# Optimization experiments

Hardware: AMD Instinct MI355X
Metric: run time of the kernel (lower is better)

## Reference

```python
import jax, jax.numpy as jnp
import numpy as np

N = 50000      # nodes
E = 800000     # edges (before self-loops)
DIN = 128
DH = 16        # per-head channels, layer 1
H = 8          # heads, layer 1
DOUT = 128     # layer 2 output (heads=1)
EDIM = 8       # edge_attr dim (unused by math: edge_dim=None in GATConv)
EPS_BN = 1e-5
NEG_SLOPE = 0.2


def _gat_conv(x, edge_index, W, a_src, a_dst, bias, heads, ch):
    """PyG GATConv (concat=True, add_self_loops=True, edge_dim=None)."""
    n = x.shape[0]
    loop = jnp.arange(n, dtype=edge_index.dtype)
    src = jnp.concatenate([edge_index[0], loop])  # [E+N]
    dst = jnp.concatenate([edge_index[1], loop])
    h = (x @ W).reshape(n, heads, ch)             # [N,H,C]
    s_src = jnp.einsum('nhc,hc->nh', h, a_src)    # [N,H]
    s_dst = jnp.einsum('nhc,hc->nh', h, a_dst)
    e = jax.nn.leaky_relu(s_src[src] + s_dst[dst], NEG_SLOPE)  # [E+N,H]
    # segment softmax over incoming edges of each dst node
    m = jax.ops.segment_max(e, dst, num_segments=n)
    ex = jnp.exp(e - m[dst])
    den = jax.ops.segment_sum(ex, dst, num_segments=n)
    alpha = ex / (den[dst] + 1e-16)               # [E+N,H]
    out = jax.ops.segment_sum(alpha[:, :, None] * h[src], dst, num_segments=n)
    return out.reshape(n, heads * ch) + bias


def _bn_selu(x, gamma, beta):
    # BatchNorm1d in training mode (batch statistics, biased variance) + SELU.
    mu = x.mean(axis=0)
    var = x.var(axis=0)
    xn = (x - mu) * jax.lax.rsqrt(var + EPS_BN)
    return jax.nn.selu(gamma * xn + beta)


def setup_inputs() -> dict:
    key = jax.random.key(0)
    ks = jax.random.split(key, 12)
    x = jax.random.normal(ks[0], (N, DIN), jnp.float32)
    edge_index = jax.random.randint(ks[1], (2, E), 0, N, jnp.int32)
    edge_attr = jax.random.normal(ks[2], (E, EDIM), jnp.float32)
    W1 = jax.random.normal(ks[3], (DIN, H * DH), jnp.float32) / np.sqrt(DIN)
    a_src1 = jax.random.normal(ks[4], (H, DH), jnp.float32) / np.sqrt(DH)
    a_dst1 = jax.random.normal(ks[5], (H, DH), jnp.float32) / np.sqrt(DH)
    b1 = jnp.zeros((H * DH,), jnp.float32)
    g1 = jnp.ones((H * DH,), jnp.float32)
    beta1 = jnp.zeros((H * DH,), jnp.float32)
    W2 = jax.random.normal(ks[6], (H * DH, DOUT), jnp.float32) / np.sqrt(H * DH)
    a_src2 = jax.random.normal(ks[7], (1, DOUT), jnp.float32) / np.sqrt(DOUT)
    a_dst2 = jax.random.normal(ks[8], (1, DOUT), jnp.float32) / np.sqrt(DOUT)
    b2 = jnp.zeros((DOUT,), jnp.float32)
    g2 = jnp.ones((DOUT,), jnp.float32)
    beta2 = jnp.zeros((DOUT,), jnp.float32)
    return dict(x=x, edge_index=edge_index, edge_attr=edge_attr,
                W1=W1, a_src1=a_src1, a_dst1=a_dst1, b1=b1, g1=g1, beta1=beta1,
                W2=W2, a_src2=a_src2, a_dst2=a_dst2, b2=b2, g2=g2, beta2=beta2)


def reference(x, edge_index, edge_attr,
              W1, a_src1, a_dst1, b1, g1, beta1,
              W2, a_src2, a_dst2, b2, g2, beta2):
    # edge_attr is unused: GATConv built with edge_dim=None ignores edge features.
    h = _gat_conv(x, edge_index, W1, a_src1, a_dst1, b1, H, DH)   # [N, H*DH]
    h = _bn_selu(h, g1, beta1)                                    # dropout = identity (eval)
    h = _gat_conv(h, edge_index, W2, a_src2, a_dst2, b2, 1, DOUT) # [N, DOUT]
    h = _bn_selu(h, g2, beta2)
    return h
```

## Files before the change

kernel.cpp:

```cpp
#include <hip/hip_runtime.h>

#define SELU_SCALE 1.0507009873554805f
#define SELU_ALPHA 1.6732632423543772f

typedef __attribute__((ext_vector_type(8))) short short8;
typedef __attribute__((ext_vector_type(4))) float f32x4;

#define BCAP 20480

static __device__ __forceinline__ float leaky02(float v) {
  return v > 0.0f ? v : 0.2f * v;
}

static __device__ __forceinline__ ushort f2bf(float f) {
  uint b = __float_as_uint(f);
  return (ushort)((b + 0x7fffu + ((b >> 16) & 1u)) >> 16);
}
static __device__ __forceinline__ float bf2f(ushort u) {
  return __uint_as_float(((uint)u) << 16);
}

static __device__ __forceinline__ float selu_f(float y) {
  return y > 0.f ? SELU_SCALE * y : SELU_SCALE * SELU_ALPHA * (__expf(y) - 1.f);
}

__global__ __launch_bounds__(256) void pack_kernel(const float* __restrict__ W1,
                                                   const float* __restrict__ W2,
                                                   ushort* __restrict__ Wp1,
                                                   ushort* __restrict__ Wp2) {
  int idx = blockIdx.x * 256 + threadIdx.x;
  const float* W = (idx < 16384) ? W1 : W2;
  ushort* Wp = (idx < 16384) ? Wp1 : Wp2;
  int t = idx & 16383;
  int b = t & 7, i = (t >> 3) & 15, g = (t >> 7) & 3, kt = (t >> 9) & 3, ct = t >> 11;
  int k = kt * 32 + g * 8 + b, col = ct * 16 + i;
  Wp[t] = f2bf(W[k * 128 + col]);
}

template <int HEADS, bool BN>
__global__ __launch_bounds__(256) void gemm_mfma_kernel(
    const float* __restrict__ X, const ushort* __restrict__ Wp, ushort* __restrict__ H,
    const float* __restrict__ asr, const float* __restrict__ adt,
    float* __restrict__ ssrc, float* __restrict__ sdst, int n,
    const float* __restrict__ stats, const float* __restrict__ gamma,
    const float* __restrict__ beta) {
  __shared__ float sc[128], sh[128];
  if (BN) {
    int t = threadIdx.x;
    if (t < 128) {
      float invN = 1.0f / (float)n;
      float mu = stats[t] * invN;
      float var = stats[128 + t] * invN - mu * mu;
      float rs = rsqrtf(var + 1e-5f);
      float s = gamma[t] * rs;
      sc[t] = s;
      sh[t] = beta[t] - s * mu;
    }
    __syncthreads();
  }
  const int tid = threadIdx.x;
  const int w = tid >> 6, l = tid & 63;
  const int lj = l & 15, lg = l >> 4;
  const int row = blockIdx.x * 64 + w * 16 + lj;
  const bool rowok = row < n;
  const float* xrow = X + (size_t)row * 128;

  f32x4 acc[8];
#pragma unroll
  for (int ct = 0; ct < 8; ++ct) acc[ct] = (f32x4){0.f, 0.f, 0.f, 0.f};

#pragma unroll
  for (int kt = 0; kt < 4; ++kt) {
    const int k0 = kt * 32 + lg * 8;
    float4 xa = make_float4(0.f, 0.f, 0.f, 0.f), xb = xa;
    if (rowok) {
      xa = *(const float4*)(xrow + k0);
      xb = *(const float4*)(xrow + k0 + 4);
    }
    float xv[8] = {xa.x, xa.y, xa.z, xa.w, xb.x, xb.y, xb.z, xb.w};
    if (BN) {
#pragma unroll
      for (int b = 0; b < 8; ++b) xv[b] = selu_f(xv[b] * sc[k0 + b] + sh[k0 + b]);
    }
    short8 bx;
#pragma unroll
    for (int b = 0; b < 8; ++b) bx[b] = (short)f2bf(xv[b]);
#pragma unroll
    for (int ct = 0; ct < 8; ++ct) {
      short8 af = *(const short8*)(Wp + ((((ct * 4 + kt) * 4 + lg) * 16 + lj) << 3));
      acc[ct] = __builtin_amdgcn_mfma_f32_16x16x32_bf16(af, bx, acc[ct], 0, 0, 0);
    }
  }

  if (rowok) {
#pragma unroll
    for (int ct = 0; ct < 8; ++ct) {
      ushort4 h4;
      h4.x = f2bf(acc[ct][0]);
      h4.y = f2bf(acc[ct][1]);
      h4.z = f2bf(acc[ct][2]);
      h4.w = f2bf(acc[ct][3]);
      *(ushort4*)&H[(size_t)row * 128 + ct * 16 + lg * 4] = h4;
    }
  }

  if (HEADS == 8) {
    float ps[8], pd[8];
#pragma unroll
    for (int ct = 0; ct < 8; ++ct) {
      float4 av = *(const float4*)&asr[ct * 16 + lg * 4];
      float4 dv = *(const float4*)&adt[ct * 16 + lg * 4];
      ps[ct] = acc[ct][0] * av.x + acc[ct][1] * av.y + acc[ct][2] * av.z + acc[ct][3] * av.w;
      pd[ct] = acc[ct][0] * dv.x + acc[ct][1] * dv.y + acc[ct][2] * dv.z + acc[ct][3] * dv.w;
      ps[ct] += __shfl_xor(ps[ct], 16);
      ps[ct] += __shfl_xor(ps[ct], 32);
      pd[ct] += __shfl_xor(pd[ct], 16);
      pd[ct] += __shfl_xor(pd[ct], 32);
    }
    if (lg == 0 && rowok) {
      *(float4*)&ssrc[(size_t)row * 8] = make_float4(ps[0], ps[1], ps[2], ps[3]);
      *(float4*)&ssrc[(size_t)row * 8 + 4] = make_float4(ps[4], ps[5], ps[6], ps[7]);
      *(float4*)&sdst[(size_t)row * 8] = make_float4(pd[0], pd[1], pd[2], pd[3]);
      *(float4*)&sdst[(size_t)row * 8 + 4] = make_float4(pd[4], pd[5], pd[6], pd[7]);
    }
  } else {
    float ps = 0.f, pd = 0.f;
#pragma unroll
    for (int ct = 0; ct < 8; ++ct) {
      float4 av = *(const float4*)&asr[ct * 16 + lg * 4];
      float4 dv = *(const float4*)&adt[ct * 16 + lg * 4];
      ps += acc[ct][0] * av.x + acc[ct][1] * av.y + acc[ct][2] * av.z + acc[ct][3] * av.w;
      pd += acc[ct][0] * dv.x + acc[ct][1] * dv.y + acc[ct][2] * dv.z + acc[ct][3] * dv.w;
    }
    ps += __shfl_xor(ps, 16);
    ps += __shfl_xor(ps, 32);
    pd += __shfl_xor(pd, 16);
    pd += __shfl_xor(pd, 32);
    if (lg == 0 && rowok) {
      ssrc[row] = ps;
      sdst[row] = pd;
    }
  }
}

__global__ __launch_bounds__(256) void bucket_kernel(const int* __restrict__ ei,
                                                     int* __restrict__ gcur,
                                                     uint* __restrict__ bucket,
                                                     int nE, int EA, int NB) {
  __shared__ int lcnt[64];
  __shared__ int lbase[64];
  int tid = threadIdx.x;
  if (tid < 64) lcnt[tid] = 0;
  __syncthreads();
  int e0 = blockIdx.x * 1024;
  uint ent[4];
  int bk[4], lp[4];
#pragma unroll
  for (int j = 0; j < 4; ++j) {
    int e = e0 + j * 256 + tid;
    bk[j] = -1;
    if (e < EA) {
      int src, dst;
      if (e < nE) {
        src = ei[e];
        dst = ei[nE + e];
      } else {
        src = dst = e - nE;
      }
      bk[j] = dst >> 10;
      ent[j] = ((uint)src << 10) | (uint)(dst & 1023);
      lp[j] = atomicAdd(&lcnt[bk[j]], 1);
    }
  }
  __syncthreads();
  if (tid < NB && lcnt[tid] > 0) lbase[tid] = atomicAdd(&gcur[tid], lcnt[tid]);
  __syncthreads();
#pragma unroll
  for (int j = 0; j < 4; ++j) {
    if (bk[j] >= 0) bucket[(size_t)bk[j] * BCAP + lbase[bk[j]] + lp[j]] = ent[j];
  }
}

__global__ __launch_bounds__(1024) void csrbuild_kernel(const int* __restrict__ gcur,
                                                        const uint* __restrict__ bucket,
                                                        int* __restrict__ offs,
                                                        int* __restrict__ csr,
                                                        int n, int NB) {
  __shared__ int ldeg[1024];
  __shared__ int loff[1024];
  __shared__ int lwsum[16];
  __shared__ int sbase;
  int b = blockIdx.x, tid = threadIdx.x;
  int lane = tid & 63, w = tid >> 6;
  if (tid < 64) {
    int v = (tid < NB) ? gcur[tid] : 0;
    int x = v;
#pragma unroll
    for (int s = 1; s < 64; s <<= 1) {
      int t = __shfl_up(x, s);
      if (tid >= s) x += t;
    }
    if (tid == b) sbase = x - v;
  }
  ldeg[tid] = 0;
  __syncthreads();
  int base = sbase;
  int cnt = gcur[b];
  const uint* bb = bucket + (size_t)b * BCAP;
  for (int k = tid; k < cnt; k += 1024) atomicAdd(&ldeg[bb[k] & 1023], 1);
  __syncthreads();
  int v = ldeg[tid];
  int x = v;
#pragma unroll
  for (int s = 1; s < 64; s <<= 1) {
    int t = __shfl_up(x, s);
    if (lane >= s) x += t;
  }
  if (lane == 63) lwsum[w] = x;
  __syncthreads();
  if (w == 0 && lane < 16) {
    int wv = lwsum[lane];
    int y = wv;
#pragma unroll
    for (int s = 1; s < 16; s <<= 1) {
      int t = __shfl_up(y, s);
      if (lane >= s) y += t;
    }
    lwsum[lane] = y - wv;
  }
  __syncthreads();
  int excl = x - v + lwsum[w];
  loff[tid] = excl;
  int node = b * 1024 + tid;
  if (node < n) offs[node] = base + excl;
  if (b == NB - 1 && tid == 0) offs[n] = base + cnt;
  __syncthreads();
  ldeg[tid] = loff[tid];
  __syncthreads();
  for (int k = tid; k < cnt; k += 1024) {
    uint e = bb[k];
    int pos = atomicAdd(&ldeg[e & 1023], 1);
    csr[base + pos] = (int)(e >> 10);
  }
}

__global__ __launch_bounds__(256) void agg1_kernel(const ushort* __restrict__ h1,
                                                   const int* __restrict__ csr,
                                                   const int* __restrict__ offs,
                                                   const float* __restrict__ ssrc,
                                                   const float* __restrict__ sdst,
                                                   const float* __restrict__ bias,
                                                   float* __restrict__ out, int nN) {
  int wid = (blockIdx.x * blockDim.x + threadIdx.x) >> 6;
  int lane = threadIdx.x & 63;
  int half = lane >> 5, ll = lane & 31;
  if (wid >= nN) return;
  int c = ll * 4;
  int h = ll >> 2;
  float sd = sdst[wid * 8 + h];
  int beg = offs[wid];
  int deg = offs[wid + 1] - beg;
  float a0 = 0.f, a1 = 0.f, a2 = 0.f, a3 = 0.f, den = 0.f;
  int i = half;
  for (; i + 6 < deg; i += 8) {
    int s0 = csr[beg + i];
    int s1 = csr[beg + i + 2];
    int s2 = csr[beg + i + 4];
    int s3 = csr[beg + i + 6];
    float e0 = ssrc[s0 * 8 + h];
    float e1 = ssrc[s1 * 8 + h];
    float e2 = ssrc[s2 * 8 + h];
    float e3 = ssrc[s3 * 8 + h];
    ushort4 u0 = *(const ushort4*)&h1[(size_t)s0 * 128 + c];
    ushort4 u1 = *(const ushort4*)&h1[(size_t)s1 * 128 + c];
    ushort4 u2 = *(const ushort4*)&h1[(size_t)s2 * 128 + c];
    ushort4 u3 = *(const ushort4*)&h1[(size_t)s3 * 128 + c];
    float A0 = __expf(leaky02(e0 + sd));
    float A1 = __expf(leaky02(e1 + sd));
    float A2 = __expf(leaky02(e2 + sd));
    float A3 = __expf(leaky02(e3 + sd));
    a0 += A0 * bf2f(u0.x) + A1 * bf2f(u1.x) + A2 * bf2f(u2.x) + A3 * bf2f(u3.x);
    a1 += A0 * bf2f(u0.y) + A1 * bf2f(u1.y) + A2 * bf2f(u2.y) + A3 * bf2f(u3.y);
    a2 += A0 * bf2f(u0.z) + A1 * bf2f(u1.z) + A2 * bf2f(u2.z) + A3 * bf2f(u3.z);
    a3 += A0 * bf2f(u0.w) + A1 * bf2f(u1.w) + A2 * bf2f(u2.w) + A3 * bf2f(u3.w);
    den += (A0 + A1) + (A2 + A3);
  }
  for (; i < deg; i += 2) {
    int s0 = csr[beg + i];
    float e0 = ssrc[s0 * 8 + h];
    ushort4 u0 = *(const ushort4*)&h1[(size_t)s0 * 128 + c];
    float A0 = __expf(leaky02(e0 + sd));
    a0 += A0 * bf2f(u0.x);
    a1 += A0 * bf2f(u0.y);
    a2 += A0 * bf2f(u0.z);
    a3 += A0 * bf2f(u0.w);
    den += A0;
  }
  a0 += __shfl_xor(a0, 32);
  a1 += __shfl_xor(a1, 32);
  a2 += __shfl_xor(a2, 32);
  a3 += __shfl_xor(a3, 32);
  den += __shfl_xor(den, 32);
  if (half == 0) {
    float invd = 1.0f / (den + 1e-16f);
    float4 bv = *(const float4*)&bias[c];
    *(float4*)&out[(size_t)wid * 128 + c] =
        make_float4(a0 * invd + bv.x, a1 * invd + bv.y, a2 * invd + bv.z, a3 * invd + bv.w);
  }
}

__global__ __launch_bounds__(256) void agg2_kernel(const ushort* __restrict__ h2,
                                                   const int* __restrict__ csr,
                                                   const int* __restrict__ offs,
                                                   const float* __restrict__ ssrc,
                                                   const float* __restrict__ sdst,
                                                   const float* __restrict__ bias,
                                                   float* __restrict__ out, int nN) {
  int wid = (blockIdx.x * blockDim.x + threadIdx.x) >> 6;
  int lane = threadIdx.x & 63;
  int half = lane >> 5, ll = lane & 31;
  if (wid >= nN) return;
  int c = ll * 4;
  float sd = sdst[wid];
  int beg = offs[wid];
  int deg = offs[wid + 1] - beg;
  float a0 = 0.f, a1 = 0.f, a2 = 0.f, a3 = 0.f, den = 0.f;
  int i = half;
  for (; i + 6 < deg; i += 8) {
    int s0 = csr[beg + i];
    int s1 = csr[beg + i + 2];
    int s2 = csr[beg + i + 4];
    int s3 = csr[beg + i + 6];
    float e0 = ssrc[s0];
    float e1 = ssrc[s1];
    float e2 = ssrc[s2];
    float e3 = ssrc[s3];
    ushort4 u0 = *(const ushort4*)&h2[(size_t)s0 * 128 + c];
    ushort4 u1 = *(const ushort4*)&h2[(size_t)s1 * 128 + c];
    ushort4 u2 = *(const ushort4*)&h2[(size_t)s2 * 128 + c];
    ushort4 u3 = *(const ushort4*)&h2[(size_t)s3 * 128 + c];
    float A0 = __expf(leaky02(e0 + sd));
    float A1 = __expf(leaky02(e1 + sd));
    float A2 = __expf(leaky02(e2 + sd));
    float A3 = __expf(leaky02(e3 + sd));
    a0 += A0 * bf2f(u0.x) + A1 * bf2f(u1.x) + A2 * bf2f(u2.x) + A3 * bf2f(u3.x);
    a1 += A0 * bf2f(u0.y) + A1 * bf2f(u1.y) + A2 * bf2f(u2.y) + A3 * bf2f(u3.y);
    a2 += A0 * bf2f(u0.z) + A1 * bf2f(u1.z) + A2 * bf2f(u2.z) + A3 * bf2f(u3.z);
    a3 += A0 * bf2f(u0.w) + A1 * bf2f(u1.w) + A2 * bf2f(u2.w) + A3 * bf2f(u3.w);
    den += (A0 + A1) + (A2 + A3);
  }
  for (; i < deg; i += 2) {
    int s0 = csr[beg + i];
    float e0 = ssrc[s0];
    ushort4 u0 = *(const ushort4*)&h2[(size_t)s0 * 128 + c];
    float A0 = __expf(leaky02(e0 + sd));
    a0 += A0 * bf2f(u0.x);
    a1 += A0 * bf2f(u0.y);
    a2 += A0 * bf2f(u0.z);
    a3 += A0 * bf2f(u0.w);
    den += A0;
  }
  a0 += __shfl_xor(a0, 32);
  a1 += __shfl_xor(a1, 32);
  a2 += __shfl_xor(a2, 32);
  a3 += __shfl_xor(a3, 32);
  den += __shfl_xor(den, 32);
  if (half == 0) {
    float invd = 1.0f / (den + 1e-16f);
    float4 bv = *(const float4*)&bias[c];
    *(float4*)&out[(size_t)wid * 128 + c] =
        make_float4(a0 * invd + bv.x, a1 * invd + bv.y, a2 * invd + bv.z, a3 * invd + bv.w);
  }
}

__global__ __launch_bounds__(256) void stats_kernel(const float* __restrict__ X,
                                                    float* __restrict__ stats, int n) {
  __shared__ float red[256];
  int tid = threadIdx.x;
  int c = tid & 127;
  int half = tid >> 7;
  float s = 0.f, sq = 0.f;
  int rbeg = (int)blockIdx.x * 64 + half;
  int rend = min((int)(blockIdx.x + 1) * 64, n);
#pragma unroll 4
  for (int r = rbeg; r < rend; r += 2) {
    float v = X[(size_t)r * 128 + c];
    s += v;
    sq += v * v;
  }
  red[tid] = s;
  __syncthreads();
  float s2 = (half == 0) ? s + red[tid + 128] : 0.f;
  __syncthreads();
  red[tid] = sq;
  __syncthreads();
  if (half == 0) {
    float sq2 = sq + red[tid + 128];
    atomicAdd(&stats[c], s2);
    atomicAdd(&stats[128 + c], sq2);
  }
}

__global__ __launch_bounds__(256) void bnselu_kernel(const float* __restrict__ X,
                                                     const float* __restrict__ stats,
                                                     const float* __restrict__ gamma,
                                                     const float* __restrict__ beta,
                                                     float* __restrict__ Y, int n) {
  int gid = blockIdx.x * blockDim.x + threadIdx.x;
  if (gid >= n * 32) return;
  int c = (gid & 31) * 4;
  int r = gid >> 5;
  float invN = 1.0f / (float)n;
  float4 x = *(const float4*)&X[(size_t)r * 128 + c];
  float o[4];
#pragma unroll
  for (int j = 0; j < 4; ++j) {
    float xx = (j == 0) ? x.x : (j == 1) ? x.y : (j == 2) ? x.z : x.w;
    float mu = stats[c + j] * invN;
    float var = stats[128 + c + j] * invN - mu * mu;
    float rs = rsqrtf(var + 1e-5f);
    float y = gamma[c + j] * ((xx - mu) * rs) + beta[c + j];
    o[j] = selu_f(y);
  }
  *(float4*)&Y[(size_t)r * 128 + c] = make_float4(o[0], o[1], o[2], o[3]);
}

extern "C" void kernel_launch(void* const* d_in, const int* in_sizes, int n_in,
                              void* d_out, int out_size, void* d_ws, size_t ws_size,
                              hipStream_t stream) {
  const float* x   = (const float*)d_in[0];
  const int*   ei  = (const int*)d_in[1];
  const float* W1  = (const float*)d_in[3];
  const float* as1 = (const float*)d_in[4];
  const float* ad1 = (const float*)d_in[5];
  const float* b1  = (const float*)d_in[6];
  const float* g1  = (const float*)d_in[7];
  const float* be1 = (const float*)d_in[8];
  const float* W2  = (const float*)d_in[9];
  const float* as2 = (const float*)d_in[10];
  const float* ad2 = (const float*)d_in[11];
  const float* b2  = (const float*)d_in[12];
  const float* g2  = (const float*)d_in[13];
  const float* be2 = (const float*)d_in[14];
  float* out = (float*)d_out;

  const int n  = in_sizes[0] / 128;
  const int nE = in_sizes[1] / 2;
  const int EA = nE + n;
  const int NB = (n + 1023) >> 10;

  float* ws = (float*)d_ws;
  size_t o = 0;
  float* Bf = ws + o;     o += (size_t)n * 128;
  ushort* H = (ushort*)(ws + o); o += (size_t)n * 64;
  float* ssrc1 = ws + o;  o += (size_t)n * 8;
  float* sdst1 = ws + o;  o += (size_t)n * 8;
  float* ssrc2 = ws + o;  o += n;
  float* sdst2 = ws + o;  o += n;
  ushort* Wp1 = (ushort*)(ws + o); o += 8192;
  ushort* Wp2 = (ushort*)(ws + o); o += 8192;
  float* zbase = ws + o;
  float* stats1 = ws + o; o += 256;
  float* stats2 = ws + o; o += 256;
  int* gcur = (int*)(ws + o); o += 64;
  size_t zwords = (size_t)((ws + o) - zbase);
  int* offs = (int*)(ws + o); o += (size_t)n + 1;
  int* csr  = (int*)(ws + o); o += EA;
  uint* bucket = (uint*)(ws + o); o += (size_t)NB * BCAP;

  hipMemsetAsync(zbase, 0, zwords * sizeof(float), stream);

  bucket_kernel<<<(EA + 1023) / 1024, 256, 0, stream>>>(ei, gcur, bucket, nE, EA, NB);
  csrbuild_kernel<<<NB, 1024, 0, stream>>>(gcur, bucket, offs, csr, n, NB);
  pack_kernel<<<128, 256, 0, stream>>>(W1, W2, Wp1, Wp2);

  gemm_mfma_kernel<8, false><<<(n + 63) / 64, 256, 0, stream>>>(
      x, Wp1, H, as1, ad1, ssrc1, sdst1, n, nullptr, nullptr, nullptr);
  agg1_kernel<<<(n + 3) / 4, 256, 0, stream>>>(H, csr, offs, ssrc1, sdst1, b1, Bf, n);
  stats_kernel<<<(n + 63) / 64, 256, 0, stream>>>(Bf, stats1, n);

  gemm_mfma_kernel<1, true><<<(n + 63) / 64, 256, 0, stream>>>(
      Bf, Wp2, H, as2, ad2, ssrc2, sdst2, n, stats1, g1, be1);
  agg2_kernel<<<(n + 3) / 4, 256, 0, stream>>>(H, csr, offs, ssrc2, sdst2, b2, out, n);
  stats_kernel<<<(n + 63) / 64, 256, 0, stream>>>(out, stats2, n);
  bnselu_kernel<<<(n * 32 + 255) / 256, 256, 0, stream>>>(out, stats2, g2, be2, out, n);
}
```

Before: 233.3 us.

## Fuse weight packing into bucket kernel, split GEMM columns across waves, deepen gather unroll

Weight packing now runs in extra blocks of the edge-bucketing kernel, which removes one launch. The GEMM now gives each wave half the output columns of a 16-row tile (32 rows per block), so the grid doubles and each wave holds fewer accumulators. For the single-head layer the attention scores are combined with float atomics, which means ssrc2/sdst2 had to move into the zeroed workspace region. The aggregation loops now batch 8 neighbours per step instead of 4 to expose more memory-level parallelism, at the cost of higher register pressure.

Result: slower. 258.2 us (+10.7%).

```diff
diff --git a/kernel.cpp b/kernel.cpp
--- a/kernel.cpp
+++ b/kernel.cpp
@@ -24,17 +24,116 @@
   return y > 0.f ? SELU_SCALE * y : SELU_SCALE * SELU_ALPHA * (__expf(y) - 1.f);
 }
 
-__global__ __launch_bounds__(256) void pack_kernel(const float* __restrict__ W1,
-                                                   const float* __restrict__ W2,
-                                                   ushort* __restrict__ Wp1,
-                                                   ushort* __restrict__ Wp2) {
-  int idx = blockIdx.x * 256 + threadIdx.x;
-  const float* W = (idx < 16384) ? W1 : W2;
-  ushort* Wp = (idx < 16384) ? Wp1 : Wp2;
-  int t = idx & 16383;
-  int b = t & 7, i = (t >> 3) & 15, g = (t >> 7) & 3, kt = (t >> 9) & 3, ct = t >> 11;
-  int k = kt * 32 + g * 8 + b, col = ct * 16 + i;
-  Wp[t] = f2bf(W[k * 128 + col]);
+__global__ __launch_bounds__(256) void bucketpack_kernel(
+    const int* __restrict__ ei, int* __restrict__ gcur, uint* __restrict__ bucket,
+    const float* __restrict__ W1, const float* __restrict__ W2,
+    ushort* __restrict__ Wp1, ushort* __restrict__ Wp2,
+    int nE, int EA, int NB, int nbb) {
+  int tid = threadIdx.x;
+  if (blockIdx.x >= nbb) {
+    int idx = (blockIdx.x - nbb) * 256 + tid;
+    const float* W = (idx < 16384) ? W1 : W2;
+    ushort* Wp = (idx < 16384) ? Wp1 : Wp2;
+    int t = idx & 16383;
+    int b = t & 7, i = (t >> 3) & 15, g = (t >> 7) & 3, kt = (t >> 9) & 3, ct = t >> 11;
+    int k = kt * 32 + g * 8 + b, col = ct * 16 + i;
+    Wp[t] = f2bf(W[k * 128 + col]);
+    return;
+  }
+  __shared__ int lcnt[64];
+  __shared__ int lbase[64];
+  if (tid < 64) lcnt[tid] = 0;
+  __syncthreads();
+  int e0 = blockIdx.x * 1024;
+  uint ent[4];
+  int bk[4], lp[4];
+#pragma unroll
+  for (int j = 0; j < 4; ++j) {
+    int e = e0 + j * 256 + tid;
+    bk[j] = -1;
+    if (e < EA) {
+      int src, dst;
+      if (e < nE) {
+        src = ei[e];
+        dst = ei[nE + e];
+      } else {
+        src = dst = e - nE;
+      }
+      bk[j] = dst >> 10;
+      ent[j] = ((uint)src << 10) | (uint)(dst & 1023);
+      lp[j] = atomicAdd(&lcnt[bk[j]], 1);
+    }
+  }
+  __syncthreads();
+  if (tid < NB && lcnt[tid] > 0) lbase[tid] = atomicAdd(&gcur[tid], lcnt[tid]);
+  __syncthreads();
+#pragma unroll
+  for (int j = 0; j < 4; ++j) {
+    if (bk[j] >= 0) bucket[(size_t)bk[j] * BCAP + lbase[bk[j]] + lp[j]] = ent[j];
+  }
+}
+
+__global__ __launch_bounds__(1024) void csrbuild_kernel(const int* __restrict__ gcur,
+                                                        const uint* __restrict__ bucket,
+                                                        int* __restrict__ offs,
+                                                        int* __restrict__ csr,
+                                                        int n, int NB) {
+  __shared__ int ldeg[1024];
+  __shared__ int loff[1024];
+  __shared__ int lwsum[16];
+  __shared__ int sbase;
+  int b = blockIdx.x, tid = threadIdx.x;
+  int lane = tid & 63, w = tid >> 6;
+  if (tid < 64) {
+    int v = (tid < NB) ? gcur[tid] : 0;
+    int x = v;
+#pragma unroll
+    for (int s = 1; s < 64; s <<= 1) {
+      int t = __shfl_up(x, s);
+      if (tid >= s) x += t;
+    }
+    if (tid == b) sbase = x - v;
+  }
+  ldeg[tid] = 0;
+  __syncthreads();
+  int base = sbase;
+  int cnt = gcur[b];
+  const uint* bb = bucket + (size_t)b * BCAP;
+  for (int k = tid; k < cnt; k += 1024) atomicAdd(&ldeg[bb[k] & 1023], 1);
+  __syncthreads();
+  int v = ldeg[tid];
+  int x = v;
+#pragma unroll
+  for (int s = 1; s < 64; s <<= 1) {
+    int t = __shfl_up(x, s);
+    if (lane >= s) x += t;
+  }
+  if (lane == 63) lwsum[w] = x;
+  __syncthreads();
+  if (w == 0 && lane < 16) {
+    int wv = lwsum[lane];
+    int y = wv;
+#pragma unroll
+    for (int s = 1; s < 16; s <<= 1) {
+      int t = __shfl_up(y, s);
+      if (lane >= s) y += t;
+    }
+    lwsum[lane] = y - wv;
+  }
+  __syncthreads();
+  int excl = x - v + lwsum[w];
+  loff[tid] = excl;
+  int node = b * 1024 + tid;
+  if (node < n) offs[node] = base + excl;
+  if (b == NB - 1 && tid == 0) offs[n] = base + cnt;
+  __syncthreads();
+  ldeg[tid] = loff[tid];
+  __syncthreads();
+  for (int k = tid; k < cnt; k += 1024) {
+    uint e = bb[k];
+    int pos = atomicAdd(&ldeg[e & 1023], 1);
+    csr[base + pos] = (int)(e >> 10);
+  }
 }
 
 template <int HEADS, bool BN>
@@ -60,14 +159,15 @@
   }
   const int tid = threadIdx.x;
   const int w = tid >> 6, l = tid & 63;
+  const int rg = w >> 1, ch = w & 1;
   const int lj = l & 15, lg = l >> 4;
-  const int row = blockIdx.x * 64 + w * 16 + lj;
+  const int row = blockIdx.x * 32 + rg * 16 + lj;
   const bool rowok = row < n;
   const float* xrow = X + (size_t)row * 128;
 
-  f32x4 acc[8];
-#pragma unroll
-  for (int ct = 0; ct < 8; ++ct) acc[ct] = (f32x4){0.f, 0.f, 0.f, 0.f};
+  f32x4 acc[4];
+#pragma unroll
+  for (int c4 = 0; c4 < 4; ++c4) acc[c4] = (f32x4){0.f, 0.f, 0.f, 0.f};
 
 #pragma unroll
   for (int kt = 0; kt < 4; ++kt) {
@@ -86,161 +186,62 @@
 #pragma unroll
     for (int b = 0; b < 8; ++b) bx[b] = (short)f2bf(xv[b]);
 #pragma unroll
-    for (int ct = 0; ct < 8; ++ct) {
+    for (int c4 = 0; c4 < 4; ++c4) {
+      int ct = ch * 4 + c4;
       short8 af = *(const short8*)(Wp + ((((ct * 4 + kt) * 4 + lg) * 16 + lj) << 3));
-      acc[ct] = __builtin_amdgcn_mfma_f32_16x16x32_bf16(af, bx, acc[ct], 0, 0, 0);
+      acc[c4] = __builtin_amdgcn_mfma_f32_16x16x32_bf16(af, bx, acc[c4], 0, 0, 0);
     }
   }
 
   if (rowok) {
 #pragma unroll
-    for (int ct = 0; ct < 8; ++ct) {
+    for (int c4 = 0; c4 < 4; ++c4) {
+      int ct = ch * 4 + c4;
       ushort4 h4;
-      h4.x = f2bf(acc[ct][0]);
-      h4.y = f2bf(acc[ct][1]);
-      h4.z = f2bf(acc[ct][2]);
-      h4.w = f2bf(acc[ct][3]);
+      h4.x = f2bf(acc[c4][0]);
+      h4.y = f2bf(acc[c4][1]);
+      h4.z = f2bf(acc[c4][2]);
+      h4.w = f2bf(acc[c4][3]);
       *(ushort4*)&H[(size_t)row * 128 + ct * 16 + lg * 4] = h4;
     }
   }
 
   if (HEADS == 8) {
-    float ps[8], pd[8];
-#pragma unroll
-    for (int ct = 0; ct < 8; ++ct) {
+    float ps[4], pd[4];
+#pragma unroll
+    for (int c4 = 0; c4 < 4; ++c4) {
+      int ct = ch * 4 + c4;
       float4 av = *(const float4*)&asr[ct * 16 + lg * 4];
       float4 dv = *(const float4*)&adt[ct * 16 + lg * 4];
-      ps[ct] = acc[ct][0] * av.x + acc[ct][1] * av.y + acc[ct][2] * av.z + acc[ct][3] * av.w;
-      pd[ct] = acc[ct][0] * dv.x + acc[ct][1] * dv.y + acc[ct][2] * dv.z + acc[ct][3] * dv.w;
-      ps[ct] += __shfl_xor(ps[ct], 16);
-      ps[ct] += __shfl_xor(ps[ct], 32);
-      pd[ct] += __shfl_xor(pd[ct], 16);
-      pd[ct] += __shfl_xor(pd[ct], 32);
+      ps[c4] = acc[c4][0] * av.x + acc[c4][1] * av.y + acc[c4][2] * av.z + acc[c4][3] * av.w;
+      pd[c4] = acc[c4][0] * dv.x + acc[c4][1] * dv.y + acc[c4][2] * dv.z + acc[c4][3] * dv.w;
+      ps[c4] += __shfl_xor(ps[c4], 16);
+      ps[c4] += __shfl_xor(ps[c4], 32);
+      pd[c4] += __shfl_xor(pd[c4], 16);
+      pd[c4] += __shfl_xor(pd[c4], 32);
     }
     if (lg == 0 && rowok) {
-      *(float4*)&ssrc[(size_t)row * 8] = make_float4(ps[0], ps[1], ps[2], ps[3]);
-      *(float4*)&ssrc[(size_t)row * 8 + 4] = make_float4(ps[4], ps[5], ps[6], ps[7]);
-      *(float4*)&sdst[(size_t)row * 8] = make_float4(pd[0], pd[1], pd[2], pd[3]);
-      *(float4*)&sdst[(size_t)row * 8 + 4] = make_float4(pd[4], pd[5], pd[6], pd[7]);
+      *(float4*)&ssrc[(size_t)row * 8 + ch * 4] = make_float4(ps[0], ps[1], ps[2], ps[3]);
+      *(float4*)&sdst[(size_t)row * 8 + ch * 4] = make_float4(pd[0], pd[1], pd[2], pd[3]);
     }
   } else {
     float ps = 0.f, pd = 0.f;
 #pragma unroll
-    for (int ct = 0; ct < 8; ++ct) {
+    for (int c4 = 0; c4 < 4; ++c4) {
+      int ct = ch * 4 + c4;
       float4 av = *(const float4*)&asr[ct * 16 + lg * 4];
       float4 dv = *(const float4*)&adt[ct * 16 + lg * 4];
-      ps += acc[ct][0] * av.x + acc[ct][1] * av.y + acc[ct][2] * av.z + acc[ct][3] * av.w;
-      pd += acc[ct][0] * dv.x + acc[ct][1] * dv.y + acc[ct][2] * dv.z + acc[ct][3] * dv.w;
+      ps += acc[c4][0] * av.x + acc[c4][1] * av.y + acc[c4][2] * av.z + acc[c4][3] * av.w;
+      pd += acc[c4][0] * dv.x + acc[c4][1] * dv.y + acc[c4][2] * dv.z + acc[c4][3] * dv.w;
     }
     ps += __shfl_xor(ps, 16);
     ps += __shfl_xor(ps, 32);
     pd += __shfl_xor(pd, 16);
     pd += __shfl_xor(pd, 32);
     if (lg == 0 && rowok) {
-      ssrc[row] = ps;
-      sdst[row] = pd;
-    }
-  }
-}
-
-__global__ __launch_bounds__(256) void bucket_kernel(const int* __restrict__ ei,
-                                                     int* __restrict__ gcur,
-                                                     uint* __restrict__ bucket,
-                                                     int nE, int EA, int NB) {
-  __shared__ int lcnt[64];
-  __shared__ int lbase[64];
-  int tid = threadIdx.x;
-  if (tid < 64) lcnt[tid] = 0;
-  __syncthreads();
-  int e0 = blockIdx.x * 1024;
-  uint ent[4];
-  int bk[4], lp[4];
-#pragma unroll
-  for (int j = 0; j < 4; ++j) {
-    int e = e0 + j * 256 + tid;
-    bk[j] = -1;
-    if (e < EA) {
-      int src, dst;
-      if (e < nE) {
-        src = ei[e];
-        dst = ei[nE + e];
-      } else {
-        src = dst = e - nE;
-      }
-      bk[j] = dst >> 10;
-      ent[j] = ((uint)src << 10) | (uint)(dst & 1023);
-      lp[j] = atomicAdd(&lcnt[bk[j]], 1);
-    }
-  }
-  __syncthreads();
-  if (tid < NB && lcnt[tid] > 0) lbase[tid] = atomicAdd(&gcur[tid], lcnt[tid]);
-  __syncthreads();
-#pragma unroll
-  for (int j = 0; j < 4; ++j) {
-    if (bk[j] >= 0) bucket[(size_t)bk[j] * BCAP + lbase[bk[j]] + lp[j]] = ent[j];
-  }
-}
-
-__global__ __launch_bounds__(1024) void csrbuild_kernel(const int* __restrict__ gcur,
-                                                        const uint* __restrict__ bucket,
-                                                        int* __restrict__ offs,
-                                                        int* __restrict__ csr,
-                                                        int n, int NB) {
-  __shared__ int ldeg[1024];
-  __shared__ int loff[1024];
-  __shared__ int lwsum[16];
-  __shared__ int sbase;
-  int b = blockIdx.x, tid = threadIdx.x;
-  int lane = tid & 63, w = tid >> 6;
-  if (tid < 64) {
-    int v = (tid < NB) ? gcur[tid] : 0;
-    int x = v;
-#pragma unroll
-    for (int s = 1; s < 64; s <<= 1) {
-      int t = __shfl_up(x, s);
-      if (tid >= s) x += t;
-    }
-    if (tid == b) sbase = x - v;
-  }
-  ldeg[tid] = 0;
-  __syncthreads();
-  int base = sbase;
-  int cnt = gcur[b];
-  const uint* bb = bucket + (size_t)b * BCAP;
-  for (int k = tid; k < cnt; k += 1024) atomicAdd(&ldeg[bb[k] & 1023], 1);
-  __syncthreads();
-  int v = ldeg[tid];
-  int x = v;
-#pragma unroll
-  for (int s = 1; s < 64; s <<= 1) {
-    int t = __shfl_up(x, s);
-    if (lane >= s) x += t;
-  }
-  if (lane == 63) lwsum[w] = x;
-  __syncthreads();
-  if (w == 0 && lane < 16) {
-    int wv = lwsum[lane];
-    int y = wv;
-#pragma unroll
-    for (int s = 1; s < 16; s <<= 1) {
-      int t = __shfl_up(y, s);
-      if (lane >= s) y += t;
-    }
-    lwsum[lane] = y - wv;
-  }
-  __syncthreads();
-  int excl = x - v + lwsum[w];
-  loff[tid] = excl;
-  int node = b * 1024 + tid;
-  if (node < n) offs[node] = base + excl;
-  if (b == NB - 1 && tid == 0) offs[n] = base + cnt;
-  __syncthreads();
-  ldeg[tid] = loff[tid];
-  __syncthreads();
-  for (int k = tid; k < cnt; k += 1024) {
-    uint e = bb[k];
-    int pos = atomicAdd(&ldeg[e & 1023], 1);
-    csr[base + pos] = (int)(e >> 10);
+      atomicAdd(&ssrc[row], ps);
+      atomicAdd(&sdst[row], pd);
+    }
   }
 }
 
@@ -262,28 +263,27 @@
   int deg = offs[wid + 1] - beg;
   float a0 = 0.f, a1 = 0.f, a2 = 0.f, a3 = 0.f, den = 0.f;
   int i = half;
-  for (; i + 6 < deg; i += 8) {
-    int s0 = csr[beg + i];
-    int s1 = csr[beg + i + 2];
-    int s2 = csr[beg + i + 4];
-    int s3 = csr[beg + i + 6];
-    float e0 = ssrc[s0 * 8 + h];
-    float e1 = ssrc[s1 * 8 + h];
-    float e2 = ssrc[s2 * 8 + h];
-    float e3 = ssrc[s3 * 8 + h];
-    ushort4 u0 = *(const ushort4*)&h1[(size_t)s0 * 128 + c];
-    ushort4 u1 = *(const ushort4*)&h1[(size_t)s1 * 128 + c];
-    ushort4 u2 = *(const ushort4*)&h1[(size_t)s2 * 128 + c];
-    ushort4 u3 = *(const ushort4*)&h1[(size_t)s3 * 128 + c];
-    float A0 = __expf(leaky02(e0 + sd));
-    float A1 = __expf(leaky02(e1 + sd));
-    float A2 = __expf(leaky02(e2 + sd));
-    float A3 = __expf(leaky02(e3 + sd));
-    a0 += A0 * bf2f(u0.x) + A1 * bf2f(u1.x) + A2 * bf2f(u2.x) + A3 * bf2f(u3.x);
-    a1 += A0 * bf2f(u0.y) + A1 * bf2f(u1.y) + A2 * bf2f(u2.y) + A3 * bf2f(u3.y);
-    a2 += A0 * bf2f(u0.z) + A1 * bf2f(u1.z) + A2 * bf2f(u2.z) + A3 * bf2f(u3.z);
-    a3 += A0 * bf2f(u0.w) + A1 * bf2f(u1.w) + A2 * bf2f(u2.w) + A3 * bf2f(u3.w);
-    den += (A0 + A1) + (A2 + A3);
+  for (; i + 14 < deg; i += 16) {
+    int s[8];
+    float e[8];
+    ushort4 u[8];
+    float A[8];
+#pragma unroll
+    for (int j = 0; j < 8; ++j) s[j] = csr[beg + i + 2 * j];
+#pragma unroll
+    for (int j = 0; j < 8; ++j) e[j] = ssrc[s[j] * 8 + h];
+#pragma unroll
+    for (int j = 0; j < 8; ++j) u[j] = *(const ushort4*)&h1[(size_t)s[j] * 128 + c];
+#pragma unroll
+    for (int j = 0; j < 8; ++j) A[j] = __expf(leaky02(e[j] + sd));
+#pragma unroll
+    for (int j = 0; j < 8; ++j) {
+      a0 += A[j] * bf2f(u[j].x);
+      a1 += A[j] * bf2f(u[j].y);
+      a2 += A[j] * bf2f(u[j].z);
+      a3 += A[j] * bf2f(u[j].w);
+      den += A[j];
+    }
   }
   for (; i < deg; i += 2) {
     int s0 = csr[beg + i];
@@ -326,28 +326,27 @@
   int deg = offs[wid + 1] - beg;
   float a0 = 0.f, a1 = 0.f, a2 = 0.f, a3 = 0.f, den = 0.f;
   int i = half;
-  for (; i + 6 < deg; i += 8) {
-    int s0 = csr[beg + i];
-    int s1 = csr[beg + i + 2];
-    int s2 = csr[beg + i + 4];
-    int s3 = csr[beg + i + 6];
-    float e0 = ssrc[s0];
-    float e1 = ssrc[s1];
-    float e2 = ssrc[s2];
-    float e3 = ssrc[s3];
-    ushort4 u0 = *(const ushort4*)&h2[(size_t)s0 * 128 + c];
-    ushort4 u1 = *(const ushort4*)&h2[(size_t)s1 * 128 + c];
-    ushort4 u2 = *(const ushort4*)&h2[(size_t)s2 * 128 + c];
-    ushort4 u3 = *(const ushort4*)&h2[(size_t)s3 * 128 + c];
-    float A0 = __expf(leaky02(e0 + sd));
-    float A1 = __expf(leaky02(e1 + sd));
-    float A2 = __expf(leaky02(e2 + sd));
-    float A3 = __expf(leaky02(e3 + sd));
-    a0 += A0 * bf2f(u0.x) + A1 * bf2f(u1.x) + A2 * bf2f(u2.x) + A3 * bf2f(u3.x);
-    a1 += A0 * bf2f(u0.y) + A1 * bf2f(u1.y) + A2 * bf2f(u2.y) + A3 * bf2f(u3.y);
-    a2 += A0 * bf2f(u0.z) + A1 * bf2f(u1.z) + A2 * bf2f(u2.z) + A3 * bf2f(u3.z);
-    a3 += A0 * bf2f(u0.w) + A1 * bf2f(u1.w) + A2 * bf2f(u2.w) + A3 * bf2f(u3.w);
-    den += (A0 + A1) + (A2 + A3);
+  for (; i + 14 < deg; i += 16) {
+    int s[8];
+    float e[8];
+    ushort4 u[8];
+    float A[8];
+#pragma unroll
+    for (int j = 0; j < 8; ++j) s[j] = csr[beg + i + 2 * j];
+#pragma unroll
+    for (int j = 0; j < 8; ++j) e[j] = ssrc[s[j]];
+#pragma unroll
+    for (int j = 0; j < 8; ++j) u[j] = *(const ushort4*)&h2[(size_t)s[j] * 128 + c];
+#pragma unroll
+    for (int j = 0; j < 8; ++j) A[j] = __expf(leaky02(e[j] + sd));
+#pragma unroll
+    for (int j = 0; j < 8; ++j) {
+      a0 += A[j] * bf2f(u[j].x);
+      a1 += A[j] * bf2f(u[j].y);
+      a2 += A[j] * bf2f(u[j].z);
+      a3 += A[j] * bf2f(u[j].w);
+      den += A[j];
+    }
   }
   for (; i < deg; i += 2) {
     int s0 = csr[beg + i];
@@ -448,6 +447,7 @@
   const int nE = in_sizes[1] / 2;
   const int EA = nE + n;
   const int NB = (n + 1023) >> 10;
+  const int nbb = (EA + 1023) / 1024;
 
   float* ws = (float*)d_ws;
   size_t o = 0;
@@ -455,14 +455,14 @@
   ushort* H = (ushort*)(ws + o); o += (size_t)n * 64;
   float* ssrc1 = ws + o;  o += (size_t)n * 8;
   float* sdst1 = ws + o;  o += (size_t)n * 8;
-  float* ssrc2 = ws + o;  o += n;
-  float* sdst2 = ws + o;  o += n;
   ushort* Wp1 = (ushort*)(ws + o); o += 8192;
   ushort* Wp2 = (ushort*)(ws + o); o += 8192;
   float* zbase = ws + o;
   float* stats1 = ws + o; o += 256;
   float* stats2 = ws + o; o += 256;
   int* gcur = (int*)(ws + o); o += 64;
+  float* ssrc2 = ws + o;  o += n;
+  float* sdst2 = ws + o;  o += n;
   size_t zwords = (size_t)((ws + o) - zbase);
   int* offs = (int*)(ws + o); o += (size_t)n + 1;
   int* csr  = (int*)(ws + o); o += EA;
@@ -470,16 +470,16 @@
 
   hipMemsetAsync(zbase, 0, zwords * sizeof(float), stream);
 
-  bucket_kernel<<<(EA + 1023) / 1024, 256, 0, stream>>>(ei, gcur, bucket, nE, EA, NB);
+  bucketpack_kernel<<<nbb + 128, 256, 0, stream>>>(ei, gcur, bucket, W1, W2, Wp1, Wp2,
+                                                   nE, EA, NB, nbb);
   csrbuild_kernel<<<NB, 1024, 0, stream>>>(gcur, bucket, offs, csr, n, NB);
-  pack_kernel<<<128, 256, 0, stream>>>(W1, W2, Wp1, Wp2);
-
-  gemm_mfma_kernel<8, false><<<(n + 63) / 64, 256, 0, stream>>>(
+
+  gemm_mfma_kernel<8, false><<<(n + 31) / 32, 256, 0, stream>>>(
       x, Wp1, H, as1, ad1, ssrc1, sdst1, n, nullptr, nullptr, nullptr);
   agg1_kernel<<<(n + 3) / 4, 256, 0, stream>>>(H, csr, offs, ssrc1, sdst1, b1, Bf, n);
   stats_kernel<<<(n + 63) / 64, 256, 0, stream>>>(Bf, stats1, n);
 
-  gemm_mfma_kernel<1, true><<<(n + 63) / 64, 256, 0, stream>>>(
+  gemm_mfma_kernel<1, true><<<(n + 31) / 32, 256, 0, stream>>>(
       Bf, Wp2, H, as2, ad2, ssrc2, sdst2, n, stats1, g1, be1);
   agg2_kernel<<<(n + 3) / 4, 256, 0, stream>>>(H, csr, offs, ssrc2, sdst2, b2, out, n);
   stats_kernel<<<(n + 63) / 64, 256, 0, stream>>>(out, stats2, n);
```
